# Kernel tuning notes

Measured on AMD Instinct MI355X. Metric: run time of the kernel, lower is better.

## Reference

```python
import jax, jax.numpy as jnp
import numpy as np

B, T, C, H, DFF = 4, 1024, 1024, 16, 4096
HS = C // H  # 64
EPS = 1e-5


def layer_norm(x, g, b):
    mu = jnp.mean(x, axis=-1, keepdims=True)
    var = jnp.var(x, axis=-1, keepdims=True)
    return (x - mu) * jax.lax.rsqrt(var + EPS) * g + b


def setup_inputs() -> dict:
    key = jax.random.key(0)
    ks = jax.random.split(key, 12)
    s = 0.02
    return {
        "x": jax.random.normal(ks[0], (B, T, C), jnp.float32),
        "wq": jax.random.normal(ks[1], (H, C, HS), jnp.float32) * s,
        "wk": jax.random.normal(ks[2], (H, C, HS), jnp.float32) * s,
        "wv": jax.random.normal(ks[3], (H, C, HS), jnp.float32) * s,
        "w_proj": jax.random.normal(ks[4], (H * HS, C), jnp.float32) * s,
        "b_proj": jnp.zeros((C,), jnp.float32),
        "w1": jax.random.normal(ks[5], (C, DFF), jnp.float32) * s,
        "b1": jnp.zeros((DFF,), jnp.float32),
        "w2": jax.random.normal(ks[6], (DFF, C), jnp.float32) * s,
        "b2": jnp.zeros((C,), jnp.float32),
        "g1": jnp.ones((C,), jnp.float32),
        "be1": jnp.zeros((C,), jnp.float32),
        "g2": jnp.ones((C,), jnp.float32),
        "be2": jnp.zeros((C,), jnp.float32),
    }


def reference(x, wq, wk, wv, w_proj, b_proj, w1, b1, w2, b2, g1, be1, g2, be2):
    h = layer_norm(x, g1, be1)
    # per-head projections, vectorized over heads: [B,H,T,HS]
    q = jnp.einsum('btc,hcd->bhtd', h, wq)
    k = jnp.einsum('btc,hcd->bhtd', h, wk)
    v = jnp.einsum('btc,hcd->bhtd', h, wv)
    # mask=None in the original forward, so no causal masking
    wei = jnp.einsum('bhtd,bhsd->bhts', q, k) * (HS ** -0.5)
    wei = jax.nn.softmax(wei, axis=-1)  # [B,H,T,T]
    out = jnp.einsum('bhts,bhsd->bhtd', wei, v)
    out = out.transpose(0, 2, 1, 3).reshape(B, T, H * HS)  # concat heads
    attn_out = out @ w_proj + b_proj
    x = x + attn_out
    h2 = layer_norm(x, g2, be2)
    ff = jax.nn.relu(h2 @ w1 + b1) @ w2 + b2
    x = x + ff
    return x, wei
```

## Files before the change

### kernel.cpp

```cpp
#include <hip/hip_runtime.h>
#include <hip/hip_bf16.h>

#define BB    4
#define TT    1024
#define CC    1024
#define HH    16
#define HSZ   64
#define DFF   4096
#define NTOK  (BB*TT)
#define BHN   (BB*HH)

typedef __attribute__((ext_vector_type(8))) short bf16x8;
typedef __attribute__((ext_vector_type(4))) float f32x4;

#define VMC0  asm volatile("s_waitcnt vmcnt(0)" ::: "memory")
#define VMC2  asm volatile("s_waitcnt vmcnt(2)" ::: "memory")
#define LGK0  asm volatile("s_waitcnt lgkmcnt(0)" ::: "memory")
#define BARRIER do { asm volatile("" ::: "memory"); \
                     __builtin_amdgcn_s_barrier();  \
                     asm volatile("" ::: "memory"); } while (0)

#define QSCALE 0.18033688f

__device__ __forceinline__ ushort f2b(float v) {
    union { float f; unsigned u; } c; c.f = v;
    unsigned r = c.u + 0x7fffu + ((c.u >> 16) & 1u);
    return (ushort)(r >> 16);
}
__device__ __forceinline__ void stv(float* p, float v)  { *p = v; }
__device__ __forceinline__ void stv(ushort* p, float v) { *p = f2b(v); }

__device__ __forceinline__ void gload16(const void* g, void* l) {
    __builtin_amdgcn_global_load_lds(
        (const __attribute__((address_space(1))) void*)g,
        (__attribute__((address_space(3))) void*)l, 16, 0, 0);
}

__global__ __launch_bounds__(256)
void ln_k(const float* __restrict__ x, const float* __restrict__ g,
          const float* __restrict__ be, ushort* __restrict__ o)
{
    __shared__ float s1[4], s2[4];
    long row = blockIdx.x;
    const float4* xr = (const float4*)(x + row * CC);
    float4 v = xr[threadIdx.x];
    float a = v.x + v.y + v.z + v.w;
    float b = v.x*v.x + v.y*v.y + v.z*v.z + v.w*v.w;
    for (int off = 32; off > 0; off >>= 1) {
        a += __shfl_down(a, off);
        b += __shfl_down(b, off);
    }
    if ((threadIdx.x & 63) == 0) { s1[threadIdx.x >> 6] = a; s2[threadIdx.x >> 6] = b; }
    __syncthreads();
    float sum = s1[0] + s1[1] + s1[2] + s1[3];
    float sq  = s2[0] + s2[1] + s2[2] + s2[3];
    float mu  = sum * (1.0f / CC);
    float var = sq * (1.0f / CC) - mu * mu;
    float inv = rsqrtf(var + 1e-5f);
    float4 gg = ((const float4*)g)[threadIdx.x];
    float4 bb = ((const float4*)be)[threadIdx.x];
    ushort4 r;
    r.x = f2b((v.x - mu) * inv * gg.x + bb.x);
    r.y = f2b((v.y - mu) * inv * gg.y + bb.y);
    r.z = f2b((v.z - mu) * inv * gg.z + bb.z);
    r.w = f2b((v.w - mu) * inv * gg.w + bb.w);
    ((ushort4*)(o + row * CC))[threadIdx.x] = r;
}

__global__ __launch_bounds__(256)
void cvtall_k(const float* __restrict__ wq, const float* __restrict__ wk,
              const float* __restrict__ wv, const float* __restrict__ wproj,
              const float* __restrict__ w1, const float* __restrict__ w2,
              ushort* __restrict__ wqkvT, ushort* __restrict__ wpT,
              ushort* __restrict__ w1T, ushort* __restrict__ w2T)
{
    __shared__ float t[32][33];
    int idx = blockIdx.x;
    const float* src; ushort* dst; int R, Cc, bx, by;
    if (idx < 3072) {
        int seg = idx >> 10, rem = idx & 1023;
        int z = rem >> 6, tt2 = rem & 63;
        src = (seg == 0 ? wq : seg == 1 ? wk : wv) + (long)z * 65536;
        dst = wqkvT + (long)seg * (1L << 20) + (long)z * 65536;
        R = 1024; Cc = 64; bx = tt2 & 1; by = tt2 >> 1;
    } else if (idx < 4096) {
        int tt2 = idx - 3072;
        src = wproj; dst = wpT; R = 1024; Cc = 1024; bx = tt2 & 31; by = tt2 >> 5;
    } else if (idx < 8192) {
        int tt2 = idx - 4096;
        src = w1; dst = w1T; R = 1024; Cc = 4096; bx = tt2 & 127; by = tt2 >> 7;
    } else {
        int tt2 = idx - 8192;
        src = w2; dst = w2T; R = 4096; Cc = 1024; bx = tt2 & 31; by = tt2 >> 5;
    }
    int r0 = by * 32, c0 = bx * 32;
    int tx = threadIdx.x & 31, ty = threadIdx.x >> 5;
#pragma unroll
    for (int i = 0; i < 4; i++)
        t[ty + 8*i][tx] = src[(long)(r0 + ty + 8*i) * Cc + c0 + tx];
    __syncthreads();
#pragma unroll
    for (int i = 0; i < 4; i++)
        dst[(long)(c0 + ty + 8*i) * R + r0 + tx] = f2b(t[tx][ty + 8*i]);
}

enum { OL_PLAIN = 0, OL_QKV3 = 1 };
constexpr int EBIAS = 1, ERELU = 2, ERES = 4, ESCALE = 8;

template<int BM, int BN, int WM, int WN, int OL, int EPI, typename OutT>
__global__ __launch_bounds__(256)
void mgemm_k(const ushort* __restrict__ A, const ushort* __restrict__ Bt,
             const float* __restrict__ bias, const float* __restrict__ res,
             OutT* __restrict__ C, int M, int N, int K,
             long sA, long sB, long sC, float scale)
{
    constexpr int BK = 64;
    constexpr int FM = BM / WM / 16, FN = BN / WN / 16;
    __shared__ ushort As[BM * BK];
    __shared__ ushort Bs[BN * BK];
    const int tid = threadIdx.x;
    const int w = tid >> 6, l = tid & 63;
    const int wr = w / WN, wc = w % WN;
    const int l15 = l & 15, l4 = l >> 4;
    const int bh = blockIdx.z;
    const ushort* Ap = A  + (long)bh * sA + (long)(blockIdx.y * BM) * K;
    const ushort* Bp = Bt + (long)bh * sB + (long)(blockIdx.x * BN) * K;

    f32x4 acc[FM][FN];
#pragma unroll
    for (int m = 0; m < FM; m++)
#pragma unroll
        for (int n = 0; n < FN; n++) acc[m][n] = (f32x4){0.f, 0.f, 0.f, 0.f};

    const int arow = tid >> 3;
    const int achk = tid & 7;

    for (int k0 = 0; k0 < K; k0 += BK) {
#pragma unroll
        for (int i = 0; i < BM / 32; i++)
            gload16(Ap + (long)(i*32 + arow) * K + k0 + achk*8,
                    &As[(i*32 + w*8) * BK]);
#pragma unroll
        for (int i = 0; i < BN / 32; i++)
            gload16(Bp + (long)(i*32 + arow) * K + k0 + achk*8,
                    &Bs[(i*32 + w*8) * BK]);
        __syncthreads();
#pragma unroll
        for (int kk = 0; kk < 2; kk++) {
            const int ko = kk*32 + l4*8;
            bf16x8 af[FM], bfr[FN];
#pragma unroll
            for (int m = 0; m < FM; m++)
                af[m] = *(const bf16x8*)&As[(wr*(BM/WM) + m*16 + l15) * BK + ko];
#pragma unroll
            for (int n = 0; n < FN; n++)
                bfr[n] = *(const bf16x8*)&Bs[(wc*(BN/WN) + n*16 + l15) * BK + ko];
#pragma unroll
            for (int m = 0; m < FM; m++)
#pragma unroll
                for (int n = 0; n < FN; n++)
                    acc[m][n] = __builtin_amdgcn_mfma_f32_16x16x32_bf16(
                        af[m], bfr[n], acc[m][n], 0, 0, 0);
        }
        __syncthreads();
    }

#pragma unroll
    for (int m = 0; m < FM; m++) {
        int rbase = blockIdx.y*BM + wr*(BM/WM) + m*16 + l4*4;
#pragma unroll
        for (int n = 0; n < FN; n++) {
            int col = blockIdx.x*BN + wc*(BN/WN) + n*16 + l15;
#pragma unroll
            for (int r = 0; r < 4; r++) {
                int row = rbase + r;
                float v = acc[m][n][r];
                if (EPI & ESCALE) v *= scale;
                if (EPI & EBIAS)  v += bias[col];
                if (EPI & ERELU)  v = fmaxf(v, 0.f);
                if (EPI & ERES)   v += res[(long)row * N + col];
                long idx;
                if (OL == OL_PLAIN) {
                    idx = (long)row * N + col;
                } else {
                    int seg = col >> 10;
                    int cl  = col & 1023;
                    if (seg == 0) v *= QSCALE;
                    long bh_ = ((long)((row >> 10) * HH + (cl >> 6))) * 65536;
                    long off = (seg == 2)
                        ? bh_ + (long)(cl & 63) * 1024 + (row & 1023)
                        : bh_ + (long)(row & 1023) * 64 + (cl & 63);
                    idx = (long)seg * (4L << 20) + off;
                }
                stv(&C[(long)bh * sC + idx], v);
            }
        }
    }
}

__global__ __launch_bounds__(512, 2)
void fattn_k(const ushort* __restrict__ q_, const ushort* __restrict__ k_,
             const ushort* __restrict__ vt, float* __restrict__ wei,
             ushort* __restrict__ attn)
{
    __shared__ ushort Qs[256*64];
    __shared__ ushort Ks[128*64];
    __shared__ ushort Vs[64*128];
    __shared__ ushort Ps[256*128];
    float* sred = (float*)Ps;

    const int tid = threadIdx.x;
    const int w = tid >> 6, l = tid & 63;
    const int wr = w >> 1, wc = w & 1;
    const int l15 = l & 15, l4 = l >> 4;
    const int bh = blockIdx.y;
    const int q0 = blockIdx.x * 256;
    const int arow = tid >> 3, achk = tid & 7;
    const int kchk = achk ^ (arow & 7);
    const int vrow = tid >> 4;
    const int vchk = (tid & 15) ^ (vrow & 15);
    const int sw8  = (l15 & 7) << 3;
    const int sw16 = l15 << 3;

    const ushort* Qp = q_ + (long)bh * 65536;
    const ushort* Kp = k_ + (long)bh * 65536;
    const ushort* Vp = vt + (long)bh * 65536;

#pragma unroll
    for (int i = 0; i < 4; i++)
        gload16(Qp + (long)(q0 + i*64 + arow) * 64 + kchk*8, &Qs[(i*64 + w*8)*64]);
#pragma unroll
    for (int i = 0; i < 2; i++)
        gload16(Kp + (long)(i*64 + arow) * 64 + kchk*8, &Ks[(i*64 + w*8)*64]);

    float ssum[4][4];
#pragma unroll
    for (int m = 0; m < 4; m++)
#pragma unroll
        for (int r = 0; r < 4; r++) ssum[m][r] = 0.f;

    for (int st = 0; st < 8; ++st) {
        const ushort* cur = (st & 1) ? Vs : Ks;
        ushort*       nxt = (st & 1) ? Ks : Vs;
        if (st < 7) {
#pragma unroll
            for (int i = 0; i < 2; i++)
                gload16(Kp + (long)((st+1)*128 + i*64 + arow) * 64 + kchk*8,
                        &nxt[(i*64 + w*8)*64]);
            VMC2;
        } else {
            VMC0;
        }
        BARRIER;

        f32x4 sacc[4][4];
#pragma unroll
        for (int m = 0; m < 4; m++)
#pragma unroll
            for (int n = 0; n < 4; n++) sacc[m][n] = (f32x4){0.f,0.f,0.f,0.f};
        __builtin_amdgcn_s_setprio(1);
#pragma unroll
        for (int kk = 0; kk < 2; kk++) {
            const int ko = kk*32 + l4*8;
            bf16x8 af[4], bfr[4];
#pragma unroll
            for (int m = 0; m < 4; m++)
                af[m] = *(const bf16x8*)&Qs[(wr*64 + m*16 + l15)*64 + (ko ^ sw8)];
#pragma unroll
            for (int n = 0; n < 4; n++)
                bfr[n] = *(const bf16x8*)&cur[(wc*64 + n*16 + l15)*64 + (ko ^ sw8)];
#pragma unroll
            for (int m = 0; m < 4; m++)
#pragma unroll
                for (int n = 0; n < 4; n++)
                    sacc[m][n] = __builtin_amdgcn_mfma_f32_16x16x32_bf16(
                        af[m], bfr[n], sacc[m][n], 0, 0, 0);
        }
        __builtin_amdgcn_s_setprio(0);
#pragma unroll
        for (int m = 0; m < 4; m++)
#pragma unroll
            for (int r = 0; r < 4; r++) {
                float s = 0.f;
#pragma unroll
                for (int n = 0; n < 4; n++) s += exp2f(sacc[m][n][r]);
                ssum[m][r] += s;
            }
        BARRIER;
    }

#pragma unroll
    for (int i = 0; i < 2; i++)
        gload16(Kp + (long)(i*64 + arow) * 64 + kchk*8, &Ks[(i*64 + w*8)*64]);
#pragma unroll
    for (int i = 0; i < 2; i++)
        gload16(Vp + (long)(i*32 + vrow) * 1024 + vchk*8, &Vs[(i*32 + w*4)*128]);

    float linv[4][4];
#pragma unroll
    for (int m = 0; m < 4; m++)
#pragma unroll
        for (int r = 0; r < 4; r++) {
            float s = ssum[m][r];
#pragma unroll
            for (int d = 1; d < 16; d <<= 1) s += __shfl_xor(s, d);
            if (l15 == 0) sred[wc*256 + wr*64 + m*16 + l4*4 + r] = s;
        }
    LGK0; BARRIER;
#pragma unroll
    for (int m = 0; m < 4; m++)
#pragma unroll
        for (int r = 0; r < 4; r++) {
            int rg = wr*64 + m*16 + l4*4 + r;
            linv[m][r] = 1.0f / (sred[rg] + sred[256 + rg]);
        }

    f32x4 oacc[4][2];
#pragma unroll
    for (int m = 0; m < 4; m++)
#pragma unroll
        for (int n = 0; n < 2; n++) oacc[m][n] = (f32x4){0.f,0.f,0.f,0.f};

    for (int st = 0; st < 8; ++st) {
        if (st > 0) {
#pragma unroll
            for (int i = 0; i < 2; i++)
                gload16(Kp + (long)(st*128 + i*64 + arow) * 64 + kchk*8,
                        &Ks[(i*64 + w*8)*64]);
#pragma unroll
            for (int i = 0; i < 2; i++)
                gload16(Vp + (long)(i*32 + vrow) * 1024 + st*128 + vchk*8,
                        &Vs[(i*32 + w*4)*128]);
        }
        VMC0;
        BARRIER;

        f32x4 sacc[4][4];
#pragma unroll
        for (int m = 0; m < 4; m++)
#pragma unroll
            for (int n = 0; n < 4; n++) sacc[m][n] = (f32x4){0.f,0.f,0.f,0.f};
        __builtin_amdgcn_s_setprio(1);
#pragma unroll
        for (int kk = 0; kk < 2; kk++) {
            const int ko = kk*32 + l4*8;
            bf16x8 af[4], bfr[4];
#pragma unroll
            for (int m = 0; m < 4; m++)
                af[m] = *(const bf16x8*)&Qs[(wr*64 + m*16 + l15)*64 + (ko ^ sw8)];
#pragma unroll
            for (int n = 0; n < 4; n++)
                bfr[n] = *(const bf16x8*)&Ks[(wc*64 + n*16 + l15)*64 + (ko ^ sw8)];
#pragma unroll
            for (int m = 0; m < 4; m++)
#pragma unroll
                for (int n = 0; n < 4; n++)
                    sacc[m][n] = __builtin_amdgcn_mfma_f32_16x16x32_bf16(
                        af[m], bfr[n], sacc[m][n], 0, 0, 0);
        }
        __builtin_amdgcn_s_setprio(0);

        float pv[4][4][4];
#pragma unroll
        for (int m = 0; m < 4; m++)
#pragma unroll
            for (int r = 0; r < 4; r++) {
                int rg = wr*64 + m*16 + l4*4 + r;
                int psw = (rg & 15) << 3;
                float li = linv[m][r];
#pragma unroll
                for (int n = 0; n < 4; n++) {
                    int col = wc*64 + n*16 + l15;
                    float p = exp2f(sacc[m][n][r]) * li;
                    pv[m][n][r] = p;
                    Ps[rg*128 + (col ^ psw)] = f2b(p);
                }
            }
        LGK0; BARRIER;

        __builtin_amdgcn_s_setprio(1);
#pragma unroll
        for (int kc = 0; kc < 4; ++kc) {
            const int ko = kc*32 + l4*8;
            bf16x8 pa[4], vb[2];
#pragma unroll
            for (int m = 0; m < 4; m++)
                pa[m] = *(const bf16x8*)&Ps[(wr*64 + m*16 + l15)*128 + (ko ^ sw16)];
#pragma unroll
            for (int n = 0; n < 2; n++)
                vb[n] = *(const bf16x8*)&Vs[(wc*32 + n*16 + l15)*128 + (ko ^ sw16)];
#pragma unroll
            for (int m = 0; m < 4; m++)
#pragma unroll
                for (int n = 0; n < 2; n++)
                    oacc[m][n] = __builtin_amdgcn_mfma_f32_16x16x32_bf16(
                        pa[m], vb[n], oacc[m][n], 0, 0, 0);
        }
        __builtin_amdgcn_s_setprio(0);

        float* wrow = wei + (long)bh * (TT*(long)TT) + st*128;
#pragma unroll
        for (int m = 0; m < 4; m++)
#pragma unroll
            for (int r = 0; r < 4; r++) {
                int rg = wr*64 + m*16 + l4*4 + r;
#pragma unroll
                for (int n = 0; n < 4; n++) {
                    int col = wc*64 + n*16 + l15;
                    __builtin_nontemporal_store(pv[m][n][r],
                        &wrow[(long)(q0 + rg) * TT + col]);
                }
            }
        BARRIER;
    }

#pragma unroll
    for (int m = 0; m < 4; m++)
#pragma unroll
        for (int r = 0; r < 4; r++) {
            int rg = wr*64 + m*16 + l4*4 + r;
            long rowbase = ((long)(bh >> 4) * TT + q0 + rg) * CC + (long)(bh & 15) * HSZ;
#pragma unroll
            for (int n = 0; n < 2; n++)
                attn[rowbase + wc*32 + n*16 + l15] = f2b(oacc[m][n][r]);
        }
}

extern "C" void kernel_launch(void* const* d_in, const int* in_sizes, int n_in,
                              void* d_out, int out_size, void* d_ws, size_t ws_size,
                              hipStream_t stream)
{
    const float* x      = (const float*)d_in[0];
    const float* wq     = (const float*)d_in[1];
    const float* wk     = (const float*)d_in[2];
    const float* wv     = (const float*)d_in[3];
    const float* w_proj = (const float*)d_in[4];
    const float* b_proj = (const float*)d_in[5];
    const float* w1     = (const float*)d_in[6];
    const float* b1     = (const float*)d_in[7];
    const float* w2     = (const float*)d_in[8];
    const float* b2     = (const float*)d_in[9];
    const float* g1     = (const float*)d_in[10];
    const float* be1    = (const float*)d_in[11];
    const float* g2     = (const float*)d_in[12];
    const float* be2    = (const float*)d_in[13];

    float* out_x = (float*)d_out;
    float* wei   = out_x + (long)NTOK * CC;

    const long MEL = 1 << 20;
    ushort* ws16 = (ushort*)d_ws;
    ushort* h    = ws16;
    ushort* q_   = ws16 + 4*MEL;
    ushort* k_   = ws16 + 8*MEL;
    ushort* vt   = ws16 + 12*MEL;
    ushort* attn = ws16 + 16*MEL;
    ushort* h2   = ws16 + 20*MEL;
    ushort* a1   = ws16 + 24*MEL;
    ushort* wqkvT= ws16 + 40*MEL;
    ushort* w1T  = ws16 + 44*MEL;
    ushort* wpT  = ws16 + 48*MEL;
    ushort* w2T  = ws16 + 49*MEL;
    float*  x1   = (float*)(ws16 + 54*MEL);

    cvtall_k<<<12288, 256, 0, stream>>>(wq, wk, wv, w_proj, w1, w2,
                                        wqkvT, wpT, w1T, w2T);

    ln_k<<<NTOK, 256, 0, stream>>>(x, g1, be1, h);

    mgemm_k<128,128,2,2,OL_QKV3,0,ushort><<<dim3(24,32,1), 256, 0, stream>>>(
        h, wqkvT, nullptr, nullptr, q_, NTOK, 3072, CC, 0,0,0, 0.f);

    fattn_k<<<dim3(4, 64), 512, 0, stream>>>(q_, k_, vt, wei, attn);

    mgemm_k<128,64,2,2,OL_PLAIN,EBIAS|ERES,float><<<dim3(16,32,1), 256, 0, stream>>>(
        attn, wpT, b_proj, x, x1, NTOK, CC, CC, 0,0,0, 0.f);

    ln_k<<<NTOK, 256, 0, stream>>>(x1, g2, be2, h2);

    mgemm_k<128,128,2,2,OL_PLAIN,EBIAS|ERELU,ushort><<<dim3(32,32,1), 256, 0, stream>>>(
        h2, w1T, b1, nullptr, a1, NTOK, DFF, CC, 0,0,0, 0.f);

    mgemm_k<128,64,2,2,OL_PLAIN,EBIAS|ERES,float><<<dim3(16,32,1), 256, 0, stream>>>(
        a1, w2T, b2, x1, out_x, NTOK, CC, DFF, 0,0,0, 0.f);
}
```

Measured before the change: 349.2 us.

## Give each wave full key width and keep Q fragments in registers

Changes the attention kernel's warp tiling so each of the 8 waves owns 32 query rows across all 128 key columns, rather than a 4x2 grid of 64x64 tiles. Q fragments are loaded once from global memory into registers, which removes the Q shared-memory buffer and its per-step LDS reads. Each wave now holds complete rows, so the row-sum reduction needs only shuffles, and the shared-memory cross-wave reduction and one barrier before the PV product are dropped. In exchange each wave reads the whole K/V tile from LDS, and Q is loaded directly without coalescing through LDS.

Measured after the change: 343.4 us, median of 2. Within noise of the previous version (-1.7%).

```diff
diff --git a/kernel.cpp b/kernel.cpp
--- a/kernel.cpp
+++ b/kernel.cpp
@@ -203,15 +203,12 @@
              const ushort* __restrict__ vt, float* __restrict__ wei,
              ushort* __restrict__ attn)
 {
-    __shared__ ushort Qs[256*64];
     __shared__ ushort Ks[128*64];
     __shared__ ushort Vs[64*128];
     __shared__ ushort Ps[256*128];
-    float* sred = (float*)Ps;
 
     const int tid = threadIdx.x;
     const int w = tid >> 6, l = tid & 63;
-    const int wr = w >> 1, wc = w & 1;
     const int l15 = l & 15, l4 = l >> 4;
     const int bh = blockIdx.y;
     const int q0 = blockIdx.x * 256;
@@ -227,15 +224,20 @@
     const ushort* Vp = vt + (long)bh * 65536;
 
 #pragma unroll
-    for (int i = 0; i < 4; i++)
-        gload16(Qp + (long)(q0 + i*64 + arow) * 64 + kchk*8, &Qs[(i*64 + w*8)*64]);
-#pragma unroll
     for (int i = 0; i < 2; i++)
         gload16(Kp + (long)(i*64 + arow) * 64 + kchk*8, &Ks[(i*64 + w*8)*64]);
 
-    float ssum[4][4];
-#pragma unroll
-    for (int m = 0; m < 4; m++)
+    bf16x8 qf[2][2];
+#pragma unroll
+    for (int m = 0; m < 2; m++)
+#pragma unroll
+        for (int kk = 0; kk < 2; kk++)
+            qf[m][kk] = *(const bf16x8*)
+                &Qp[(long)(q0 + w*32 + m*16 + l15)*64 + kk*32 + l4*8];
+
+    float ssum[2][4];
+#pragma unroll
+    for (int m = 0; m < 2; m++)
 #pragma unroll
         for (int r = 0; r < 4; r++) ssum[m][r] = 0.f;
 
@@ -253,37 +255,34 @@
         }
         BARRIER;
 
-        f32x4 sacc[4][4];
-#pragma unroll
-        for (int m = 0; m < 4; m++)
-#pragma unroll
-            for (int n = 0; n < 4; n++) sacc[m][n] = (f32x4){0.f,0.f,0.f,0.f};
+        f32x4 sacc[2][8];
+#pragma unroll
+        for (int m = 0; m < 2; m++)
+#pragma unroll
+            for (int n = 0; n < 8; n++) sacc[m][n] = (f32x4){0.f,0.f,0.f,0.f};
         __builtin_amdgcn_s_setprio(1);
 #pragma unroll
         for (int kk = 0; kk < 2; kk++) {
             const int ko = kk*32 + l4*8;
-            bf16x8 af[4], bfr[4];
-#pragma unroll
-            for (int m = 0; m < 4; m++)
-                af[m] = *(const bf16x8*)&Qs[(wr*64 + m*16 + l15)*64 + (ko ^ sw8)];
-#pragma unroll
-            for (int n = 0; n < 4; n++)
-                bfr[n] = *(const bf16x8*)&cur[(wc*64 + n*16 + l15)*64 + (ko ^ sw8)];
-#pragma unroll
-            for (int m = 0; m < 4; m++)
-#pragma unroll
-                for (int n = 0; n < 4; n++)
+            bf16x8 bfr[8];
+#pragma unroll
+            for (int n = 0; n < 8; n++)
+                bfr[n] = *(const bf16x8*)&cur[(n*16 + l15)*64 + (ko ^ sw8)];
+#pragma unroll
+            for (int m = 0; m < 2; m++)
+#pragma unroll
+                for (int n = 0; n < 8; n++)
                     sacc[m][n] = __builtin_amdgcn_mfma_f32_16x16x32_bf16(
-                        af[m], bfr[n], sacc[m][n], 0, 0, 0);
+                        qf[m][kk], bfr[n], sacc[m][n], 0, 0, 0);
         }
         __builtin_amdgcn_s_setprio(0);
 #pragma unroll
-        for (int m = 0; m < 4; m++)
+        for (int m = 0; m < 2; m++)
 #pragma unroll
             for (int r = 0; r < 4; r++) {
                 float s = 0.f;
 #pragma unroll
-                for (int n = 0; n < 4; n++) s += exp2f(sacc[m][n][r]);
+                for (int n = 0; n < 8; n++) s += exp2f(sacc[m][n][r]);
                 ssum[m][r] += s;
             }
         BARRIER;
@@ -296,30 +295,22 @@
     for (int i = 0; i < 2; i++)
         gload16(Vp + (long)(i*32 + vrow) * 1024 + vchk*8, &Vs[(i*32 + w*4)*128]);
 
-    float linv[4][4];
-#pragma unroll
-    for (int m = 0; m < 4; m++)
+    float linv[2][4];
+#pragma unroll
+    for (int m = 0; m < 2; m++)
 #pragma unroll
         for (int r = 0; r < 4; r++) {
             float s = ssum[m][r];
 #pragma unroll
             for (int d = 1; d < 16; d <<= 1) s += __shfl_xor(s, d);
-            if (l15 == 0) sred[wc*256 + wr*64 + m*16 + l4*4 + r] = s;
-        }
-    LGK0; BARRIER;
-#pragma unroll
-    for (int m = 0; m < 4; m++)
-#pragma unroll
-        for (int r = 0; r < 4; r++) {
-            int rg = wr*64 + m*16 + l4*4 + r;
-            linv[m][r] = 1.0f / (sred[rg] + sred[256 + rg]);
-        }
-
-    f32x4 oacc[4][2];
-#pragma unroll
-    for (int m = 0; m < 4; m++)
-#pragma unroll
-        for (int n = 0; n < 2; n++) oacc[m][n] = (f32x4){0.f,0.f,0.f,0.f};
+            linv[m][r] = 1.0f / s;
+        }
+
+    f32x4 oacc[2][4];
+#pragma unroll
+    for (int m = 0; m < 2; m++)
+#pragma unroll
+        for (int n = 0; n < 4; n++) oacc[m][n] = (f32x4){0.f,0.f,0.f,0.f};
 
     for (int st = 0; st < 8; ++st) {
         if (st > 0) {
@@ -335,64 +326,61 @@
         VMC0;
         BARRIER;
 
-        f32x4 sacc[4][4];
-#pragma unroll
-        for (int m = 0; m < 4; m++)
-#pragma unroll
-            for (int n = 0; n < 4; n++) sacc[m][n] = (f32x4){0.f,0.f,0.f,0.f};
+        f32x4 sacc[2][8];
+#pragma unroll
+        for (int m = 0; m < 2; m++)
+#pragma unroll
+            for (int n = 0; n < 8; n++) sacc[m][n] = (f32x4){0.f,0.f,0.f,0.f};
         __builtin_amdgcn_s_setprio(1);
 #pragma unroll
         for (int kk = 0; kk < 2; kk++) {
             const int ko = kk*32 + l4*8;
-            bf16x8 af[4], bfr[4];
-#pragma unroll
-            for (int m = 0; m < 4; m++)
-                af[m] = *(const bf16x8*)&Qs[(wr*64 + m*16 + l15)*64 + (ko ^ sw8)];
-#pragma unroll
-            for (int n = 0; n < 4; n++)
-                bfr[n] = *(const bf16x8*)&Ks[(wc*64 + n*16 + l15)*64 + (ko ^ sw8)];
-#pragma unroll
-            for (int m = 0; m < 4; m++)
-#pragma unroll
-                for (int n = 0; n < 4; n++)
+            bf16x8 bfr[8];
+#pragma unroll
+            for (int n = 0; n < 8; n++)
+                bfr[n] = *(const bf16x8*)&Ks[(n*16 + l15)*64 + (ko ^ sw8)];
+#pragma unroll
+            for (int m = 0; m < 2; m++)
+#pragma unroll
+                for (int n = 0; n < 8; n++)
                     sacc[m][n] = __builtin_amdgcn_mfma_f32_16x16x32_bf16(
-                        af[m], bfr[n], sacc[m][n], 0, 0, 0);
+                        qf[m][kk], bfr[n], sacc[m][n], 0, 0, 0);
         }
         __builtin_amdgcn_s_setprio(0);
 
-        float pv[4][4][4];
-#pragma unroll
-        for (int m = 0; m < 4; m++)
+        float pv[2][8][4];
+#pragma unroll
+        for (int m = 0; m < 2; m++)
 #pragma unroll
             for (int r = 0; r < 4; r++) {
-                int rg = wr*64 + m*16 + l4*4 + r;
+                int rg = w*32 + m*16 + l4*4 + r;
                 int psw = (rg & 15) << 3;
                 float li = linv[m][r];
 #pragma unroll
-                for (int n = 0; n < 4; n++) {
-                    int col = wc*64 + n*16 + l15;
+                for (int n = 0; n < 8; n++) {
+                    int col = n*16 + l15;
                     float p = exp2f(sacc[m][n][r]) * li;
                     pv[m][n][r] = p;
                     Ps[rg*128 + (col ^ psw)] = f2b(p);
                 }
             }
-        LGK0; BARRIER;
+        LGK0;
 
         __builtin_amdgcn_s_setprio(1);
 #pragma unroll
         for (int kc = 0; kc < 4; ++kc) {
             const int ko = kc*32 + l4*8;
-            bf16x8 pa[4], vb[2];
-#pragma unroll
-            for (int m = 0; m < 4; m++)
-                pa[m] = *(const bf16x8*)&Ps[(wr*64 + m*16 + l15)*128 + (ko ^ sw16)];
-#pragma unroll
-            for (int n = 0; n < 2; n++)
-                vb[n] = *(const bf16x8*)&Vs[(wc*32 + n*16 + l15)*128 + (ko ^ sw16)];
-#pragma unroll
-            for (int m = 0; m < 4; m++)
-#pragma unroll
-                for (int n = 0; n < 2; n++)
+            bf16x8 pa[2], vb[4];
+#pragma unroll
+            for (int m = 0; m < 2; m++)
+                pa[m] = *(const bf16x8*)&Ps[(w*32 + m*16 + l15)*128 + (ko ^ sw16)];
+#pragma unroll
+            for (int n = 0; n < 4; n++)
+                vb[n] = *(const bf16x8*)&Vs[(n*16 + l15)*128 + (ko ^ sw16)];
+#pragma unroll
+            for (int m = 0; m < 2; m++)
+#pragma unroll
+                for (int n = 0; n < 4; n++)
                     oacc[m][n] = __builtin_amdgcn_mfma_f32_16x16x32_bf16(
                         pa[m], vb[n], oacc[m][n], 0, 0, 0);
         }
@@ -400,13 +388,13 @@
 
         float* wrow = wei + (long)bh * (TT*(long)TT) + st*128;
 #pragma unroll
-        for (int m = 0; m < 4; m++)
+        for (int m = 0; m < 2; m++)
 #pragma unroll
             for (int r = 0; r < 4; r++) {
-                int rg = wr*64 + m*16 + l4*4 + r;
-#pragma unroll
-                for (int n = 0; n < 4; n++) {
-                    int col = wc*64 + n*16 + l15;
+                int rg = w*32 + m*16 + l4*4 + r;
+#pragma unroll
+                for (int n = 0; n < 8; n++) {
+                    int col = n*16 + l15;
                     __builtin_nontemporal_store(pv[m][n][r],
                         &wrow[(long)(q0 + rg) * TT + col]);
                 }
@@ -415,14 +403,14 @@
     }
 
 #pragma unroll
-    for (int m = 0; m < 4; m++)
+    for (int m = 0; m < 2; m++)
 #pragma unroll
         for (int r = 0; r < 4; r++) {
-            int rg = wr*64 + m*16 + l4*4 + r;
+            int rg = w*32 + m*16 + l4*4 + r;
             long rowbase = ((long)(bh >> 4) * TT + q0 + rg) * CC + (long)(bh & 15) * HSZ;
 #pragma unroll
-            for (int n = 0; n < 2; n++)
-                attn[rowbase + wc*32 + n*16 + l15] = f2b(oacc[m][n][r]);
+            for (int n = 0; n < 4; n++)
+                attn[rowbase + n*16 + l15] = f2b(oacc[m][n][r]);
         }
 }
 
```
